# Optimization experiments

Measured on AMD Instinct MI355X. Metric: run time of the kernel, lower is better.

## Reference

```python
import jax, jax.numpy as jnp
import numpy as np

B, LAT, H, K = 8, 128, 1024, 294
N, E = 100000, 1600000
XSIZE = 128.0
TAU = 0.5
STEPS = 3


def setup_inputs() -> dict:
    key = jax.random.key(0)
    ks = jax.random.split(key, 20)
    s_in = 1.0 / np.sqrt(LAT)
    s_h = 1.0 / np.sqrt(H)
    inp = {
        "latent": jax.random.normal(ks[0], (B, LAT), jnp.float32),
        "W0": jax.random.normal(ks[1], (LAT, H), jnp.float32) * s_in,
        "b0": jnp.zeros((H,), jnp.float32),
        "W1": jax.random.normal(ks[2], (H, H), jnp.float32) * s_h,
        "b1": jnp.zeros((H,), jnp.float32),
        "W2": jax.random.normal(ks[3], (H, H), jnp.float32) * s_h,
        "b2": jnp.zeros((H,), jnp.float32),
        "W3": jax.random.normal(ks[4], (H, H), jnp.float32) * s_h,
        "b3": jnp.zeros((H,), jnp.float32),
        # coefficient heads use normal(1e-4) init in the source
        "Wx": jax.random.normal(ks[5], (H, K), jnp.float32) * 1e-4,
        "bx": jnp.zeros((K,), jnp.float32),
        "Wy": jax.random.normal(ks[6], (H, K), jnp.float32) * 1e-4,
        "by": jnp.zeros((K,), jnp.float32),
        "Wz": jax.random.normal(ks[7], (H, K), jnp.float32) * 1e-4,
        "bz": jnp.zeros((K,), jnp.float32),
        # precomputed Zernike/spherical basis evaluated at the N coords: [K, N]
        "Z": jax.random.normal(ks[8], (K, N), jnp.float32),
        "edge_weights": jax.random.uniform(ks[9], (E,), jnp.float32),
        "edge_index": jax.random.randint(ks[10], (2, E), 0, N, jnp.int64),
    }
    return inp


def _decode_coefficients(latent, W0, b0, W1, b1, W2, b2, W3, b3,
                         Wx, bx, Wy, by, Wz, bz):
    h = jax.nn.relu(latent @ W0 + b0)
    for W, b in ((W1, b1), (W2, b2), (W3, b3)):
        h = jax.nn.relu(h + h @ W + b)  # residual MLP block
    return h @ Wx + bx, h @ Wy + by, h @ Wz + bz  # [B, K] each


def _diffuse(flow, edge_index, edge_weights):
    """Graph diffusion smoothing of per-node vectors. flow: [B, N, 3]."""
    src, dst = edge_index[0], edge_index[1]
    deg = jax.ops.segment_sum(edge_weights, dst, num_segments=N)
    deg = jnp.maximum(deg, 1e-6)[:, None, None]  # [N,1,1]
    f = jnp.transpose(flow, (1, 0, 2))  # [N, B, 3]
    w = edge_weights[:, None, None]
    for _ in range(STEPS):
        msg = f[src] * w                                        # gather  [E,B,3]
        agg = jax.ops.segment_sum(msg, dst, num_segments=N)     # scatter [N,B,3]
        f = (1.0 - TAU) * f + TAU * agg / deg
    return jnp.transpose(f, (1, 0, 2))  # [B, N, 3]


def reference(latent, W0, b0, W1, b1, W2, b2, W3, b3,
              Wx, bx, Wy, by, Wz, bz, Z, edge_weights, edge_index):
    cx, cy, cz = _decode_coefficients(latent, W0, b0, W1, b1, W2, b2, W3, b3,
                                      Wx, bx, Wy, by, Wz, bz)
    # basis evaluation: per-axis coefficients contracted with Zernike basis
    dx = jnp.einsum("bk,kn->bn", cx, Z)
    dy = jnp.einsum("bk,kn->bn", cy, Z)
    dz = jnp.einsum("bk,kn->bn", cz, Z)
    flow = (0.5 * XSIZE) * jnp.stack([dx, dy, dz], axis=-1)  # [B, N, 3]
    flow = _diffuse(flow, edge_index, edge_weights)
    reg = 1e-4 * jnp.sqrt(jnp.sum(cx ** 2 + cy ** 2 + cz ** 2))
    return flow, reg
```

## Files before the change

### kernel.cpp

```cpp
#include <hip/hip_runtime.h>
#include <math.h>

#define BB 8
#define LAT 128
#define HH 1024
#define KK 294
#define NN 100000
#define EE 1600000
#define NSTEPS 3
#define XS_HALF 64.0f

#define NB 391
#define FS 4
#define FCH 74
#define FNB 196
#define CS 8
#define COB 28
#define EPT 8
#define EST 200000
#define EBLK 782
#define GON 40


__device__ __forceinline__ void mlp_part_body(int bid, const float* __restrict__ hin,
                                              const float* __restrict__ W,
                                              float* __restrict__ part, int jdim) {
    int it = bid & 15;
    int bs = bid >> 4;
    int tx = threadIdx.x;
    int il = tx & 63;
    int jg = tx >> 6;
    int i = it * 64 + il;
    int j0 = bs * 64;

    __shared__ float hs[8 * 64];
    for (int u = tx; u < 512; u += 256) {
        int b = u >> 6, lj = u & 63;
        hs[u] = hin[b * jdim + j0 + lj];
    }
    __syncthreads();

    float acc[8];
#pragma unroll
    for (int b = 0; b < 8; ++b) acc[b] = 0.0f;
#pragma unroll
    for (int jj = 0; jj < 16; ++jj) {
        int lj = jg * 16 + jj;
        float w = W[(size_t)(j0 + lj) * HH + i];
#pragma unroll
        for (int b = 0; b < 8; ++b) acc[b] += hs[b * 64 + lj] * w;
    }

    __shared__ float red[4][8][64];
#pragma unroll
    for (int b = 0; b < 8; ++b) red[jg][b][il] = acc[b];
    __syncthreads();
    for (int u = tx; u < 512; u += 256) {
        int b = u >> 6, ii = u & 63;
        float s = red[0][b][ii] + red[1][b][ii] + red[2][b][ii] + red[3][b][ii];
        part[(size_t)bs * 8192 + b * HH + it * 64 + ii] = s;
    }
}

__device__ __forceinline__ void mlp_comb_body(int bid, const float* __restrict__ part,
                                              int nsplit, const float* __restrict__ resid,
                                              const float* __restrict__ bias,
                                              float* __restrict__ hout) {
    int idx = bid * 256 + threadIdx.x;
    if (idx >= BB * HH) return;
    int i = idx & (HH - 1);
    float s = bias[i];
    if (resid) s += resid[idx];
    for (int bs = 0; bs < nsplit; ++bs) s += part[(size_t)bs * 8192 + idx];
    hout[idx] = fmaxf(s, 0.0f);
}

__device__ __forceinline__ void count_body(int bid, const int* __restrict__ ei,
                                           int* __restrict__ cnt, int* __restrict__ rank) {
    int gid = bid * 256 + threadIdx.x;
    if (gid >= EST) return;
    int d[EPT];
#pragma unroll
    for (int j = 0; j < EPT; ++j) d[j] = ei[EE + gid + j * EST];
#pragma unroll
    for (int j = 0; j < EPT; ++j) {
        int p = atomicAdd(&cnt[d[j]], 1);
        rank[gid + j * EST] = p;
    }
}

__device__ __forceinline__ void bsum_body(int bid, const int* __restrict__ cnt,
                                          int* __restrict__ bsum) {
    __shared__ int red[256];
    int i = bid * 256 + threadIdx.x;
    red[threadIdx.x] = (i < NN) ? cnt[i] : 0;
    __syncthreads();
    for (int off = 128; off > 0; off >>= 1) {
        if ((int)threadIdx.x < off) red[threadIdx.x] += red[threadIdx.x + off];
        __syncthreads();
    }
    if (threadIdx.x == 0) bsum[bid] = red[0];
}

__device__ __forceinline__ void bscan_body(const int* __restrict__ bsum,
                                           int* __restrict__ bpre,
                                           int* __restrict__ offs) {
    __shared__ int A[512], Bf[512];
    int t = threadIdx.x;
    A[t] = (t < NB) ? bsum[t] : 0;
    A[t + 256] = (t + 256 < NB) ? bsum[t + 256] : 0;
    __syncthreads();
    int* s = A;
    int* d = Bf;
    for (int off = 1; off < 512; off <<= 1) {
        d[t] = s[t] + ((t >= off) ? s[t - off] : 0);
        int u = t + 256;
        d[u] = s[u] + ((u >= off) ? s[u - off] : 0);
        __syncthreads();
        int* tmp = s; s = d; d = tmp;
    }
    if (t < NB) bpre[t] = (t == 0) ? 0 : s[t - 1];
    int u = t + 256;
    if (u < NB) bpre[u] = s[u - 1];
    if (t == 0) offs[NN] = s[NB - 1];
}

__device__ __forceinline__ void offs_body(int bid, const int* __restrict__ cnt,
                                          const int* __restrict__ bpre,
                                          int* __restrict__ offs) {
    __shared__ int part[256];
    int t = threadIdx.x;
    int i = bid * 256 + t;
    int v = (i < NN) ? cnt[i] : 0;
    part[t] = v;
    __syncthreads();
    for (int off = 1; off < 256; off <<= 1) {
        int u = (t >= off) ? part[t - off] : 0;
        __syncthreads();
        part[t] += u;
        __syncthreads();
    }
    if (i < NN) offs[i] = bpre[bid] + part[t] - v;
}

__device__ __forceinline__ void fill_body(int bid, const int* __restrict__ ei,
                                          const float* __restrict__ ew,
                                          const int* __restrict__ offs,
                                          const int* __restrict__ rank,
                                          int2* __restrict__ csr) {
    int gid = bid * 256 + threadIdx.x;
    if (gid >= EST) return;
    int s[EPT], d[EPT], r[EPT];
    float w[EPT];
#pragma unroll
    for (int j = 0; j < EPT; ++j) {
        int e = gid + j * EST;
        s[j] = ei[e];
        d[j] = ei[EE + e];
        w[j] = ew[e];
        r[j] = rank[e];
    }
#pragma unroll
    for (int j = 0; j < EPT; ++j) {
        int p = offs[d[j]] + r[j];
        int2 v;
        v.x = s[j];
        v.y = __float_as_int(w[j]);
        csr[p] = v;
    }
}

__device__ __forceinline__ void degcsr_body(int bid, const int* __restrict__ offs,
                                            const int2* __restrict__ csr,
                                            float* __restrict__ invh) {
    int n = bid * 256 + threadIdx.x;
    if (n >= NN) return;
    int beg = offs[n], end = offs[n + 1];
    float s = 0.0f;
    for (int i = beg; i < end; ++i) s += __int_as_float(csr[i].y);
    invh[n] = 0.5f / fmaxf(s, 1e-6f);
}

__device__ __forceinline__ void flow_part_body(int bid, const float* __restrict__ coef,
                                               const float* __restrict__ Z,
                                               float* __restrict__ fpart) {
    int s = bid / FNB;
    int blk = bid % FNB;
    int ks = s * FCH;

    __shared__ float sc[FCH * 24];
    for (int u = threadIdx.x; u < FCH * 24; u += 256) {
        int kk = u / 24, j = u - kk * 24;
        int k = ks + kk;
        sc[u] = (k < KK) ? coef[j * KK + k] : 0.0f;
    }
    __syncthreads();

    int n0 = blk * 512 + threadIdx.x * 2;
    if (n0 >= NN) return;

    float2 acc[24];
#pragma unroll
    for (int j = 0; j < 24; ++j) acc[j] = make_float2(0.f, 0.f);

    const float4* scv = (const float4*)sc;
    for (int kk = 0; kk < FCH; ++kk) {
        int k = ks + kk;
        int kz = (k < KK) ? k : (KK - 1);
        float2 z = *(const float2*)(Z + (size_t)kz * NN + n0);
        float4 c[6];
#pragma unroll
        for (int q = 0; q < 6; ++q) c[q] = scv[kk * 6 + q];
        const float* cf = (const float*)c;
#pragma unroll
        for (int j = 0; j < 24; ++j) {
            acc[j].x += cf[j] * z.x;
            acc[j].y += cf[j] * z.y;
        }
    }

    float buf[48];
#pragma unroll
    for (int j = 0; j < 24; ++j) {
        int b = j & 7, t = j >> 3;
        buf[b * 3 + t] = acc[j].x;
        buf[24 + b * 3 + t] = acc[j].y;
    }
    float4* fr = (float4*)(fpart + (size_t)s * (NN * 24) + (size_t)n0 * 24);
#pragma unroll
    for (int q = 0; q < 12; ++q) fr[q] = ((const float4*)buf)[q];
}

__device__ __forceinline__ void flow_comb_body(int bid, float* __restrict__ fpart) {
    int idx = bid * 256 + threadIdx.x;
    if (idx >= NN * 6) return;
    float4* p0 = (float4*)fpart;
    const float4* p1 = p0 + NN * 6;
    const float4* p2 = p1 + NN * 6;
    const float4* p3 = p2 + NN * 6;
    float4 a = p0[idx], b = p1[idx], c = p2[idx], d = p3[idx];
    float4 r;
    r.x = XS_HALF * (a.x + b.x + c.x + d.x);
    r.y = XS_HALF * (a.y + b.y + c.y + d.y);
    r.z = XS_HALF * (a.z + b.z + c.z + d.z);
    r.w = XS_HALF * (a.w + b.w + c.w + d.w);
    p0[idx] = r;
}

__device__ __forceinline__ void reg_body(const float* __restrict__ coef,
                                         float* __restrict__ out_reg) {
    __shared__ float red[256];
    float s = 0.0f;
    for (int i = threadIdx.x; i < 3 * BB * KK; i += 256) {
        float v = coef[i];
        s += v * v;
    }
    red[threadIdx.x] = s;
    __syncthreads();
    for (int off = 128; off > 0; off >>= 1) {
        if ((int)threadIdx.x < off) red[threadIdx.x] += red[threadIdx.x + off];
        __syncthreads();
    }
    if (threadIdx.x == 0) out_reg[0] = 1e-4f * sqrtf(red[0]);
}


__global__ void K1_mlp0_count(const float* __restrict__ latent, const float* __restrict__ W0,
                              float* __restrict__ part, const int* __restrict__ ei,
                              int* __restrict__ cnt, int* __restrict__ rank) {
    if (blockIdx.x < 32) mlp_part_body(blockIdx.x, latent, W0, part, LAT);
    else count_body(blockIdx.x - 32, ei, cnt, rank);
}

__global__ void K2_comb0_bsum(const float* __restrict__ part, const float* __restrict__ b0,
                              float* __restrict__ hout, const int* __restrict__ cnt,
                              int* __restrict__ bsum) {
    if (blockIdx.x < 32) mlp_comb_body(blockIdx.x, part, 2, nullptr, b0, hout);
    else bsum_body(blockIdx.x - 32, cnt, bsum);
}

__global__ void K3_bscan_mlp1(const int* __restrict__ bsum, int* __restrict__ bpre,
                              int* __restrict__ offs, const float* __restrict__ hin,
                              const float* __restrict__ W1, float* __restrict__ part) {
    if (blockIdx.x == 0) bscan_body(bsum, bpre, offs);
    else mlp_part_body(blockIdx.x - 1, hin, W1, part, HH);
}

__global__ void K4_comb1_offs(const float* __restrict__ part, const float* __restrict__ resid,
                              const float* __restrict__ b1, float* __restrict__ hout,
                              const int* __restrict__ cnt, const int* __restrict__ bpre,
                              int* __restrict__ offs) {
    if (blockIdx.x < 32) mlp_comb_body(blockIdx.x, part, 16, resid, b1, hout);
    else offs_body(blockIdx.x - 32, cnt, bpre, offs);
}

__global__ void K5_mlp2_fill(const float* __restrict__ hin, const float* __restrict__ W2,
                             float* __restrict__ part, const int* __restrict__ ei,
                             const float* __restrict__ ew, const int* __restrict__ offs,
                             const int* __restrict__ rank, int2* __restrict__ csr) {
    if (blockIdx.x < 256) mlp_part_body(blockIdx.x, hin, W2, part, HH);
    else fill_body(blockIdx.x - 256, ei, ew, offs, rank, csr);
}

__global__ void K6_comb2_deg(const float* __restrict__ part, const float* __restrict__ resid,
                             const float* __restrict__ bias, float* __restrict__ hout,
                             const int* __restrict__ offs, const int2* __restrict__ csr,
                             float* __restrict__ invh) {
    if (blockIdx.x < 32) mlp_comb_body(blockIdx.x, part, 16, resid, bias, hout);
    else degcsr_body(blockIdx.x - 32, offs, csr, invh);
}

__global__ void K_mlp_part3(const float* __restrict__ hin, const float* __restrict__ W,
                            float* __restrict__ part) {
    mlp_part_body(blockIdx.x, hin, W, part, HH);
}

__global__ void K_mlp_comb(const float* __restrict__ part, const float* __restrict__ resid,
                           const float* __restrict__ bias, float* __restrict__ hout) {
    mlp_comb_body(blockIdx.x, part, 16, resid, bias, hout);
}

__global__ void k_coef_part(const float* __restrict__ h,
                            const float* __restrict__ Wx,
                            const float* __restrict__ Wy,
                            const float* __restrict__ Wz,
                            float* __restrict__ cpart) {
    int s = blockIdx.x / COB;
    int blk = blockIdx.x % COB;
    int o = blk * 256 + threadIdx.x;
    if (o >= 3 * BB * KK) return;
    int t = o / (BB * KK);
    int r = o % (BB * KK);
    int b = r / KK, k = r % KK;
    const float* W = (t == 0) ? Wx : ((t == 1) ? Wy : Wz);
    const float* hr = h + b * HH;
    int j0 = s * 128;
    float acc = 0.0f;
#pragma unroll 8
    for (int j = 0; j < 128; ++j) acc += hr[j0 + j] * W[(size_t)(j0 + j) * KK + k];
    cpart[(size_t)s * 7056 + o] = acc;
}

__global__ void k_coef_comb(const float* __restrict__ cpart,
                            const float* __restrict__ bx,
                            const float* __restrict__ by,
                            const float* __restrict__ bz,
                            float* __restrict__ coef) {
    int o = blockIdx.x * 256 + threadIdx.x;
    if (o >= 3 * BB * KK) return;
    int t = o / (BB * KK);
    int k = o % KK;
    float s = ((t == 0) ? bx : ((t == 1) ? by : bz))[k];
#pragma unroll
    for (int i = 0; i < CS; ++i) s += cpart[(size_t)i * 7056 + o];
    coef[o] = s;
}

__global__ void K11_flow_reg(const float* __restrict__ coef, const float* __restrict__ Z,
                             float* __restrict__ fpart, float* __restrict__ out_reg) {
    if (blockIdx.x < FS * FNB) flow_part_body(blockIdx.x, coef, Z, fpart);
    else reg_body(coef, out_reg);
}

__global__ void K12_fcomb(float* __restrict__ fpart) {
    flow_comb_body(blockIdx.x, fpart);
}

__global__ void k_gather(const int* __restrict__ offs, const int2* __restrict__ csr,
                         const float* __restrict__ invh,
                         const float* __restrict__ fin, float* __restrict__ fout) {
    int idx = blockIdx.x * 256 + threadIdx.x;
    if (idx >= NN * 6) return;
    int n = idx / 6;
    int q = idx - n * 6;
    int beg = offs[n], end = offs[n + 1];
    const float4* f4 = (const float4*)fin;
    float4 acc = make_float4(0.f, 0.f, 0.f, 0.f);
    for (int i = beg; i < end; ++i) {
        int2 e = csr[i];
        float w = __int_as_float(e.y);
        float4 fv = f4[(size_t)e.x * 6 + q];
        acc.x += w * fv.x;
        acc.y += w * fv.y;
        acc.z += w * fv.z;
        acc.w += w * fv.w;
    }
    float inv = invh[n];
    float4 fo = f4[(size_t)n * 6 + q];
    float4 r;
    r.x = 0.5f * fo.x + inv * acc.x;
    r.y = 0.5f * fo.y + inv * acc.y;
    r.z = 0.5f * fo.z + inv * acc.z;
    r.w = 0.5f * fo.w + inv * acc.w;
    ((float4*)fout)[(size_t)n * 6 + q] = r;
}

__global__ void k_gather_out(const int* __restrict__ offs, const int2* __restrict__ csr,
                             const float* __restrict__ invh,
                             const float* __restrict__ fin, float* __restrict__ out) {
    __shared__ float ls[GON * 24];
    int t = threadIdx.x;
    int n0 = blockIdx.x * GON;
    if (t < GON * 6) {
        int ln = t / 6, q = t - 6 * ln;
        int n = n0 + ln;
        if (n < NN) {
            int beg = offs[n], end = offs[n + 1];
            const float4* f4 = (const float4*)fin;
            float4 acc = make_float4(0.f, 0.f, 0.f, 0.f);
            for (int i = beg; i < end; ++i) {
                int2 e = csr[i];
                float w = __int_as_float(e.y);
                float4 fv = f4[(size_t)e.x * 6 + q];
                acc.x += w * fv.x;
                acc.y += w * fv.y;
                acc.z += w * fv.z;
                acc.w += w * fv.w;
            }
            float inv = invh[n];
            float4 fo = f4[(size_t)n * 6 + q];
            float* d = &ls[ln * 24 + q * 4];
            d[0] = 0.5f * fo.x + inv * acc.x;
            d[1] = 0.5f * fo.y + inv * acc.y;
            d[2] = 0.5f * fo.z + inv * acc.z;
            d[3] = 0.5f * fo.w + inv * acc.w;
        }
    }
    __syncthreads();
    int cnt = NN - n0; if (cnt > GON) cnt = GON;
    int per_b = cnt * 3;
    for (int b = 0; b < BB; ++b) {
        for (int u = t; u < per_b; u += 256) {
            int n = u / 3;
            int c = u - 3 * n;
            out[(size_t)b * (NN * 3) + (size_t)n0 * 3 + u] = ls[n * 24 + b * 3 + c];
        }
    }
}

extern "C" void kernel_launch(void* const* d_in, const int* in_sizes, int n_in,
                              void* d_out, int out_size, void* d_ws, size_t ws_size,
                              hipStream_t stream) {
    const float* latent = (const float*)d_in[0];
    const float* W0 = (const float*)d_in[1];
    const float* b0 = (const float*)d_in[2];
    const float* W1 = (const float*)d_in[3];
    const float* b1 = (const float*)d_in[4];
    const float* W2 = (const float*)d_in[5];
    const float* b2 = (const float*)d_in[6];
    const float* W3 = (const float*)d_in[7];
    const float* b3 = (const float*)d_in[8];
    const float* Wx = (const float*)d_in[9];
    const float* bx = (const float*)d_in[10];
    const float* Wy = (const float*)d_in[11];
    const float* by = (const float*)d_in[12];
    const float* Wz = (const float*)d_in[13];
    const float* bz = (const float*)d_in[14];
    const float* Z  = (const float*)d_in[15];
    const float* ew = (const float*)d_in[16];
    const int*   ei = (const int*)d_in[17];
    float* out = (float*)d_out;

    float* p = (float*)d_ws;
    float* h_a     = p; p += 8192;
    float* h_b     = p; p += 8192;
    float* hp      = p; p += 16 * 8192;
    float* coef    = p; p += 7056;
    float* cpart   = p; p += CS * 7056;
    float* invh    = p; p += 100000;
    int*   cnt     = (int*)p; p += 100000;
    int*   offs    = (int*)p; p += 100016;
    int*   bsum    = (int*)p; p += 512;
    int*   bpre    = (int*)p; p += 512;
    int*   rank    = (int*)p; p += 1600000;
    int2*  csr     = (int2*)p; p += 2 * 1600000;
    float* fpart   = p; p += (size_t)FS * NN * 24;

    hipMemsetAsync(cnt, 0, NN * sizeof(int), stream);

    K1_mlp0_count<<<32 + EBLK, 256, 0, stream>>>(latent, W0, hp, ei, cnt, rank);
    K2_comb0_bsum<<<32 + NB, 256, 0, stream>>>(hp, b0, h_a, cnt, bsum);
    K3_bscan_mlp1<<<1 + 256, 256, 0, stream>>>(bsum, bpre, offs, h_a, W1, hp);
    K4_comb1_offs<<<32 + NB, 256, 0, stream>>>(hp, h_a, b1, h_b, cnt, bpre, offs);
    K5_mlp2_fill<<<256 + EBLK, 256, 0, stream>>>(h_b, W2, hp, ei, ew, offs, rank, csr);
    K6_comb2_deg<<<32 + NB, 256, 0, stream>>>(hp, h_b, b2, h_a, offs, csr, invh);
    K_mlp_part3<<<256, 256, 0, stream>>>(h_a, W3, hp);
    K_mlp_comb<<<32, 256, 0, stream>>>(hp, h_a, b3, h_b);
    k_coef_part<<<COB * CS, 256, 0, stream>>>(h_b, Wx, Wy, Wz, cpart);
    k_coef_comb<<<COB, 256, 0, stream>>>(cpart, bx, by, bz, coef);
    K11_flow_reg<<<FS * FNB + 1, 256, 0, stream>>>(coef, Z, fpart, out + (size_t)BB * NN * 3);
    K12_fcomb<<<(NN * 6 + 255) / 256, 256, 0, stream>>>(fpart);

    float* f0 = fpart;
    float* f1 = fpart + (size_t)NN * 24;
    k_gather<<<(NN * 6 + 255) / 256, 256, 0, stream>>>(offs, csr, invh, f0, f1);
    k_gather<<<(NN * 6 + 255) / 256, 256, 0, stream>>>(offs, csr, invh, f1, f0);
    k_gather_out<<<(NN + GON - 1) / GON, 256, 0, stream>>>(offs, csr, invh, f0, out);
}
```

Before: 566.1 us.

## Fuse split-K flow basis contraction with in-block LDS reduction, drop combine kernel

Replaces the four-way split-K flow kernel plus separate combine pass with one kernel where each block's four waves split K and reduce partials through shared memory before writing scaled output directly. Coefficients are stored transposed so every wave reads a uniform coefficient row, and Z loads are software-prefetched two rows ahead. This removes the partial-buffer writes/reads and one launch, in exchange for a large shared-memory footprint per block, lower occupancy, and a serialized reduction on the first wave.

```diff
diff --git a/kernel.cpp b/kernel.cpp
--- a/kernel.cpp
+++ b/kernel.cpp
@@ -11,15 +11,14 @@
 #define XS_HALF 64.0f
 
 #define NB 391
-#define FS 4
-#define FCH 74
-#define FNB 196
 #define CS 8
 #define COB 28
 #define EPT 8
 #define EST 200000
 #define EBLK 782
 #define GON 40
+
+#define F2NB 782
 
 
 __device__ __forceinline__ void mlp_part_body(int bid, const float* __restrict__ hin,
@@ -181,70 +180,75 @@
     invh[n] = 0.5f / fmaxf(s, 1e-6f);
 }
 
-__device__ __forceinline__ void flow_part_body(int bid, const float* __restrict__ coef,
-                                               const float* __restrict__ Z,
-                                               float* __restrict__ fpart) {
-    int s = bid / FNB;
-    int blk = bid % FNB;
-    int ks = s * FCH;
-
-    __shared__ float sc[FCH * 24];
-    for (int u = threadIdx.x; u < FCH * 24; u += 256) {
-        int kk = u / 24, j = u - kk * 24;
-        int k = ks + kk;
-        sc[u] = (k < KK) ? coef[j * KK + k] : 0.0f;
-    }
-    __syncthreads();
-
-    int n0 = blk * 512 + threadIdx.x * 2;
-    if (n0 >= NN) return;
+__device__ __forceinline__ void flow2_body(int bid, const float* __restrict__ coefT,
+                                           const float* __restrict__ Z,
+                                           float* __restrict__ fout) {
+    int t = threadIdx.x;
+    int lane = t & 63;
+    int g = t >> 6;
+    int gu = __builtin_amdgcn_readfirstlane(g);
+    int kb = (gu * KK) >> 2;
+    int ke = ((gu + 1) * KK) >> 2;
+    int cnt = ke - kb;
+
+    int n0 = bid * 128;
+    int np = n0 + 2 * lane;
+    bool valid = (np + 1) < NN;
+    int npl = valid ? np : (NN - 2);
+
+    const float* crow = coefT + (size_t)kb * 24;
+    const float* zp = Z + (size_t)kb * NN + npl;
 
     float2 acc[24];
 #pragma unroll
     for (int j = 0; j < 24; ++j) acc[j] = make_float2(0.f, 0.f);
 
-    const float4* scv = (const float4*)sc;
-    for (int kk = 0; kk < FCH; ++kk) {
-        int k = ks + kk;
-        int kz = (k < KK) ? k : (KK - 1);
-        float2 z = *(const float2*)(Z + (size_t)kz * NN + n0);
-        float4 c[6];
-#pragma unroll
-        for (int q = 0; q < 6; ++q) c[q] = scv[kk * 6 + q];
-        const float* cf = (const float*)c;
+    float2 z0 = *(const float2*)zp;
+    float2 z1 = *(const float2*)(zp + NN);
+    zp += 2 * (size_t)NN;
+
+    for (int kk = 0; kk < cnt; ++kk) {
+        float2 zn = make_float2(0.f, 0.f);
+        if (kk + 2 < cnt) zn = *(const float2*)zp;
+        zp += NN;
 #pragma unroll
         for (int j = 0; j < 24; ++j) {
-            acc[j].x += cf[j] * z.x;
-            acc[j].y += cf[j] * z.y;
+            acc[j].x = fmaf(crow[j], z0.x, acc[j].x);
+            acc[j].y = fmaf(crow[j], z0.y, acc[j].y);
         }
-    }
-
-    float buf[48];
-#pragma unroll
-    for (int j = 0; j < 24; ++j) {
-        int b = j & 7, t = j >> 3;
-        buf[b * 3 + t] = acc[j].x;
-        buf[24 + b * 3 + t] = acc[j].y;
-    }
-    float4* fr = (float4*)(fpart + (size_t)s * (NN * 24) + (size_t)n0 * 24);
-#pragma unroll
-    for (int q = 0; q < 12; ++q) fr[q] = ((const float4*)buf)[q];
-}
-
-__device__ __forceinline__ void flow_comb_body(int bid, float* __restrict__ fpart) {
-    int idx = bid * 256 + threadIdx.x;
-    if (idx >= NN * 6) return;
-    float4* p0 = (float4*)fpart;
-    const float4* p1 = p0 + NN * 6;
-    const float4* p2 = p1 + NN * 6;
-    const float4* p3 = p2 + NN * 6;
-    float4 a = p0[idx], b = p1[idx], c = p2[idx], d = p3[idx];
-    float4 r;
-    r.x = XS_HALF * (a.x + b.x + c.x + d.x);
-    r.y = XS_HALF * (a.y + b.y + c.y + d.y);
-    r.z = XS_HALF * (a.z + b.z + c.z + d.z);
-    r.w = XS_HALF * (a.w + b.w + c.w + d.w);
-    p0[idx] = r;
+        crow += 24;
+        z0 = z1;
+        z1 = zn;
+    }
+
+    __shared__ float ls[3 * 64 * 50];
+    if (g > 0) {
+        float2* d = (float2*)(ls + ((g - 1) * 64 + lane) * 50);
+#pragma unroll
+        for (int j = 0; j < 24; ++j) d[j] = acc[j];
+    }
+    __syncthreads();
+    if (g == 0 && valid) {
+#pragma unroll
+        for (int s = 0; s < 3; ++s) {
+            const float2* r = (const float2*)(ls + (s * 64 + lane) * 50);
+#pragma unroll
+            for (int j = 0; j < 24; ++j) {
+                float2 v = r[j];
+                acc[j].x += v.x;
+                acc[j].y += v.y;
+            }
+        }
+        float buf[48];
+#pragma unroll
+        for (int j = 0; j < 24; ++j) {
+            buf[j] = XS_HALF * acc[j].x;
+            buf[24 + j] = XS_HALF * acc[j].y;
+        }
+        float4* fr = (float4*)(fout + (size_t)np * 24);
+#pragma unroll
+        for (int q = 0; q < 12; ++q) fr[q] = ((const float4*)buf)[q];
+    }
 }
 
 __device__ __forceinline__ void reg_body(const float* __restrict__ coef,
@@ -345,25 +349,23 @@
                             const float* __restrict__ bx,
                             const float* __restrict__ by,
                             const float* __restrict__ bz,
-                            float* __restrict__ coef) {
+                            float* __restrict__ coefT) {
     int o = blockIdx.x * 256 + threadIdx.x;
     if (o >= 3 * BB * KK) return;
     int t = o / (BB * KK);
-    int k = o % KK;
+    int r = o % (BB * KK);
+    int b = r / KK;
+    int k = r % KK;
     float s = ((t == 0) ? bx : ((t == 1) ? by : bz))[k];
 #pragma unroll
     for (int i = 0; i < CS; ++i) s += cpart[(size_t)i * 7056 + o];
-    coef[o] = s;
-}
-
-__global__ void K11_flow_reg(const float* __restrict__ coef, const float* __restrict__ Z,
-                             float* __restrict__ fpart, float* __restrict__ out_reg) {
-    if (blockIdx.x < FS * FNB) flow_part_body(blockIdx.x, coef, Z, fpart);
-    else reg_body(coef, out_reg);
-}
-
-__global__ void K12_fcomb(float* __restrict__ fpart) {
-    flow_comb_body(blockIdx.x, fpart);
+    coefT[k * 24 + b * 3 + t] = s;
+}
+
+__global__ void K11_flow_reg(const float* __restrict__ coefT, const float* __restrict__ Z,
+                             float* __restrict__ fout, float* __restrict__ out_reg) {
+    if (blockIdx.x < F2NB) flow2_body(blockIdx.x, coefT, Z, fout);
+    else reg_body(coefT, out_reg);
 }
 
 __global__ void k_gather(const int* __restrict__ offs, const int2* __restrict__ csr,
@@ -474,7 +476,7 @@
     int*   bpre    = (int*)p; p += 512;
     int*   rank    = (int*)p; p += 1600000;
     int2*  csr     = (int2*)p; p += 2 * 1600000;
-    float* fpart   = p; p += (size_t)FS * NN * 24;
+    float* fpart   = p; p += (size_t)2 * NN * 24;
 
     hipMemsetAsync(cnt, 0, NN * sizeof(int), stream);
 
@@ -488,8 +490,7 @@
     K_mlp_comb<<<32, 256, 0, stream>>>(hp, h_a, b3, h_b);
     k_coef_part<<<COB * CS, 256, 0, stream>>>(h_b, Wx, Wy, Wz, cpart);
     k_coef_comb<<<COB, 256, 0, stream>>>(cpart, bx, by, bz, coef);
-    K11_flow_reg<<<FS * FNB + 1, 256, 0, stream>>>(coef, Z, fpart, out + (size_t)BB * NN * 3);
-    K12_fcomb<<<(NN * 6 + 255) / 256, 256, 0, stream>>>(fpart);
+    K11_flow_reg<<<F2NB + 1, 256, 0, stream>>>(coef, Z, fpart, out + (size_t)BB * NN * 3);
 
     float* f0 = fpart;
     float* f1 = fpart + (size_t)NN * 24;
```

Result: no change. 559.0 us (-1.3%).
